# Kernel tuning notes

Hardware: AMD Instinct MI355X
Metric: run time of the kernel (lower is better)

The kernel has to match this reference:

```python
import jax, jax.numpy as jnp
import numpy as np
from jax import lax

D_MODEL = 1024
D_STATE = 16
D_CONV = 4
EXPAND = 2
D_INNER = EXPAND * D_MODEL
LN_EPS = 1e-5


def setup_inputs() -> dict:
    key = jax.random.key(0)
    ks = jax.random.split(key, 12)
    B, L = 4, 1024
    s = lambda fan_in: 1.0 / np.sqrt(fan_in)
    inp = {
        "x": jax.random.normal(ks[0], (B, L, D_MODEL), jnp.float32),
        # in_proj: d_model -> 2*d_inner (stored as (in, out))
        "W_in": jax.random.normal(ks[1], (D_MODEL, 2 * D_INNER), jnp.float32) * s(D_MODEL),
        "b_in": jnp.zeros((2 * D_INNER,), jnp.float32),
        # depthwise causal conv1d, kernel (d_inner, 1, d_conv)
        "conv_w": jax.random.normal(ks[2], (D_INNER, 1, D_CONV), jnp.float32) * s(D_CONV),
        "conv_b": jnp.zeros((D_INNER,), jnp.float32),
        # x_proj: d_inner -> 2*d_state
        "W_xp": jax.random.normal(ks[3], (D_INNER, 2 * D_STATE), jnp.float32) * s(D_INNER),
        "b_xp": jnp.zeros((2 * D_STATE,), jnp.float32),
        # dt_proj: d_inner -> d_inner
        "W_dt": jax.random.normal(ks[4], (D_INNER, D_INNER), jnp.float32) * s(D_INNER),
        "b_dt": jnp.zeros((D_INNER,), jnp.float32),
        # A_log = log(arange(1, d_state+1)) repeated over d_inner
        "A_log": jnp.log(jnp.broadcast_to(jnp.arange(1, D_STATE + 1, dtype=jnp.float32), (D_INNER, D_STATE))),
        "D_param": jnp.ones((D_INNER,), jnp.float32),
        # out_proj: d_inner -> d_model
        "W_out": jax.random.normal(ks[5], (D_INNER, D_MODEL), jnp.float32) * s(D_INNER),
        "b_out": jnp.zeros((D_MODEL,), jnp.float32),
        "ln_g": jnp.ones((D_MODEL,), jnp.float32),
        "ln_b": jnp.zeros((D_MODEL,), jnp.float32),
    }
    return inp


def _causal_depthwise_conv(x, w, b):
    # x: (B, d_inner, L); w: (d_inner, 1, d_conv). Left-pad d_conv-1 => causal.
    y = lax.conv_general_dilated(
        x, w, window_strides=(1,), padding=[(D_CONV - 1, 0)],
        dimension_numbers=("NCH", "OIH", "NCH"), feature_group_count=D_INNER)
    return y + b[None, :, None]


def _ssm(x, A, Bm, Cm, dt, D_param):
    # x, dt: (B,L,D)  A: (D,N)  Bm, Cm: (B,L,N)
    A_disc = jnp.exp(dt[..., None] * A)               # (B,L,D,N)
    dBx = (dt * x)[..., None] * Bm[:, :, None, :]     # (B,L,D,N) = dt*B*x_t
    h0 = jnp.zeros(x.shape[:1] + A.shape, x.dtype)    # (B,D,N)

    def step(h, inputs):
        a, bx, c = inputs                              # (B,D,N),(B,D,N),(B,N)
        h = a * h + bx
        y = jnp.einsum("bdn,bn->bd", h, c)
        return h, y

    _, ys = lax.scan(step, h0, (jnp.swapaxes(A_disc, 0, 1),
                                jnp.swapaxes(dBx, 0, 1),
                                jnp.swapaxes(Cm, 0, 1)))
    y = jnp.swapaxes(ys, 0, 1)                         # (B,L,D)
    return y + x * D_param


def reference(x, W_in, b_in, conv_w, conv_b, W_xp, b_xp, W_dt, b_dt,
              A_log, D_param, W_out, b_out, ln_g, ln_b):
    residual = x
    xr = x @ W_in + b_in                               # (B,L,2*d_inner)
    xi, res = jnp.split(xr, 2, axis=-1)
    xi = jax.nn.silu(xi)
    xi = jnp.swapaxes(xi, 1, 2)                        # (B,d_inner,L)
    xi = _causal_depthwise_conv(xi, conv_w, conv_b)
    xi = jnp.swapaxes(xi, 1, 2)
    xi = jax.nn.silu(xi)
    bc = xi @ W_xp + b_xp                              # (B,L,2*d_state)
    Bm, Cm = jnp.split(bc, 2, axis=-1)
    dt = jax.nn.softplus(xi @ W_dt + b_dt)
    A = -jnp.exp(A_log)                                # (d_inner, d_state)
    y = _ssm(xi, A, Bm, Cm, dt, D_param)
    y = y * jax.nn.silu(res)
    out = y @ W_out + b_out
    z = out + residual
    mu = jnp.mean(z, axis=-1, keepdims=True)
    var = jnp.var(z, axis=-1, keepdims=True)
    return (z - mu) * jax.lax.rsqrt(var + LN_EPS) * ln_g + ln_b
```

## Files before the change

### kernel.cpp

```cpp
#include <hip/hip_runtime.h>
#include <math.h>

#define D_MODEL 1024
#define D_INNER 2048
#define D_STATE 16
#define D_CONV  4
#define NCHUNK  16
#define LCHUNK  64

typedef unsigned short u16;
typedef __attribute__((ext_vector_type(8))) short short8;
typedef __attribute__((ext_vector_type(4))) float f32x4;
typedef __attribute__((ext_vector_type(4))) unsigned short u16x4;

__device__ __forceinline__ float silu_f(float x) { return x / (1.f + __expf(-x)); }
__device__ __forceinline__ float softplus_f(float x) {
    return fmaxf(x, 0.f) + log1pf(__expf(-fabsf(x)));
}
__device__ __forceinline__ u16 f2bf(float f) {
    union { float f; unsigned u; } c; c.f = f;
    unsigned r = c.u + 0x7fffu + ((c.u >> 16) & 1u);
    return (u16)(r >> 16);
}
__device__ __forceinline__ float bf2f(u16 v) {
    union { unsigned u; float f; } c; c.u = ((unsigned)v) << 16; return c.f;
}
__device__ __forceinline__ void gload_lds16(const void* g, void* l) {
    __builtin_amdgcn_global_load_lds((const __attribute__((address_space(1))) void*)g,
                                     (__attribute__((address_space(3))) void*)l, 16, 0, 0);
}

__global__ __launch_bounds__(256)
void f32_to_bf16_kernel(const float* __restrict__ in, u16* __restrict__ out, int n4)
{
    const int i = blockIdx.x * 256 + threadIdx.x;
    if (i >= n4) return;
    const float4 v = *(const float4*)&in[(size_t)i * 4];
    u16x4 o; o.x = f2bf(v.x); o.y = f2bf(v.y); o.z = f2bf(v.z); o.w = f2bf(v.w);
    *(u16x4*)&out[(size_t)i * 4] = o;
}

__global__ __launch_bounds__(256)
void transpose_bf16_kernel(const float* __restrict__ W, u16* __restrict__ Wt, int K, int N)
{
    __shared__ float tile[32][33];
    const int tx = threadIdx.x & 31, ty = threadIdx.x >> 5;
    const int n0 = blockIdx.x * 32, k0 = blockIdx.y * 32;
#pragma unroll
    for (int q = 0; q < 4; q++)
        tile[ty + q * 8][tx] = W[(size_t)(k0 + ty + q * 8) * N + n0 + tx];
    __syncthreads();
#pragma unroll
    for (int q = 0; q < 4; q++)
        Wt[(size_t)(n0 + ty + q * 8) * K + k0 + tx] = f2bf(tile[tx][ty + q * 8]);
}

template <int MODE>
__global__ __launch_bounds__(512, 2)
void gemm_mfma256(const u16* __restrict__ A, const u16* __restrict__ Bt,
                  const float* __restrict__ bias,
                  void* __restrict__ out0v, void* __restrict__ out1v,
                  int M, int N, int K)
{
    __shared__ __align__(16) short As[2][256 * 64];
    __shared__ __align__(16) short Bs[2][256 * 64];

    const int tid = threadIdx.x;
    const int wid = tid >> 6, lane = tid & 63;
    const int wr = wid >> 2, wc = wid & 3;
    const int row0 = blockIdx.y * 256, col0 = blockIdx.x * 256;
    const int kg = lane >> 4, r16 = lane & 15;

    f32x4 acc[8][4] = {};

    const u16* Abase = A + (size_t)row0 * K;
    const u16* Bbase = Bt + (size_t)col0 * K;

#define STAGE_A(bi, kk) do {                                                    \
        _Pragma("unroll")                                                       \
        for (int q = 0; q < 4; q++) {                                           \
            const int c = (q << 9) + tid;                                       \
            const int r = c >> 3;                                               \
            const int ks8 = (((c & 7) ^ (r & 7)) << 3);                         \
            gload_lds16(Abase + (size_t)r * K + (kk) + ks8,                     \
                        &As[bi][((q << 9) + (wid << 6)) << 3]);                 \
        }                                                                       \
    } while (0)
#define STAGE_B(bi, kk) do {                                                    \
        _Pragma("unroll")                                                       \
        for (int q = 0; q < 4; q++) {                                           \
            const int c = (q << 9) + tid;                                       \
            const int r = c >> 3;                                               \
            const int ks8 = (((c & 7) ^ (r & 7)) << 3);                         \
            gload_lds16(Bbase + (size_t)r * K + (kk) + ks8,                     \
                        &Bs[bi][((q << 9) + (wid << 6)) << 3]);                 \
        }                                                                       \
    } while (0)

    const int nt = K >> 6;
    STAGE_A(0, 0);
    STAGE_B(0, 0);

    int cur = 0;
    const int rx = r16 & 7;
    for (int t = 0; t < nt; ++t) {
        if (t + 1 < nt) {
            STAGE_A(cur ^ 1, (t + 1) << 6);
            asm volatile("s_waitcnt vmcnt(4)" ::: "memory");
        } else {
            asm volatile("s_waitcnt vmcnt(0)" ::: "memory");
        }
        __builtin_amdgcn_s_barrier();

#pragma unroll
        for (int ks = 0; ks < 2; ks++) {
            const int sl8 = (((ks << 2) + kg) ^ rx) << 3;
            short8 af[8], bg[4];
#pragma unroll
            for (int i = 0; i < 8; i++) {
                const int r = wr * 128 + i * 16 + r16;
                af[i] = *(const short8*)&As[cur][r * 64 + sl8];
            }
#pragma unroll
            for (int j = 0; j < 4; j++) {
                const int r = wc * 64 + j * 16 + r16;
                bg[j] = *(const short8*)&Bs[cur][r * 64 + sl8];
            }
            __builtin_amdgcn_s_setprio(1);
#pragma unroll
            for (int i = 0; i < 8; i++)
#pragma unroll
                for (int j = 0; j < 4; j++)
                    acc[i][j] = __builtin_amdgcn_mfma_f32_16x16x32_bf16(af[i], bg[j], acc[i][j], 0, 0, 0);
            __builtin_amdgcn_s_setprio(0);
            if (ks == 0 && t + 1 < nt)
                STAGE_B(cur ^ 1, (t + 1) << 6);
        }

        asm volatile("s_waitcnt lgkmcnt(0)" ::: "memory");
        __builtin_amdgcn_s_barrier();
        cur ^= 1;
    }
#undef STAGE_A
#undef STAGE_B

#pragma unroll
    for (int i = 0; i < 8; i++) {
#pragma unroll
        for (int j = 0; j < 4; j++) {
#pragma unroll
            for (int r = 0; r < 4; r++) {
                const int row = row0 + wr * 128 + i * 16 + kg * 4 + r;
                const int col = col0 + wc * 64 + j * 16 + r16;
                float v = acc[i][j][r] + bias[col];
                if (MODE == 0) {
                    u16* o0 = (u16*)out0v; u16* o1 = (u16*)out1v;
                    if (col < D_INNER) o0[(size_t)row * D_INNER + col] = f2bf(silu_f(v));
                    else               o1[(size_t)row * D_INNER + (col - D_INNER)] = f2bf(v);
                } else {
                    ((float*)out0v)[(size_t)row * N + col] = softplus_f(v);
                }
            }
        }
    }
}

template <int MODE>
__global__ __launch_bounds__(256)
void gemm_mfma_128(const u16* __restrict__ A, const u16* __restrict__ Bt,
                   const float* __restrict__ bias, const float* __restrict__ aux,
                   float* __restrict__ out0, int M, int N, int K)
{
    __shared__ __align__(16) short As[3][4096];
    __shared__ __align__(16) short Bs[3][4096];

    const int tid = threadIdx.x;
    const int wid = tid >> 6, lane = tid & 63;
    const int wr = wid >> 1, wc = wid & 1;
    const int row0 = blockIdx.y * 128, col0 = blockIdx.x * 128;

    f32x4 acc[4][4] = {};

    const int c0 = wid * 128 + lane;
    const int c1 = c0 + 64;
    const u16* Abase = A + (size_t)row0 * K;
    const u16* Bbase = Bt + (size_t)col0 * K;

    const int gsl8 = (((lane & 3) ^ ((lane >> 3) & 3)) << 3);
    const int kg = lane >> 4, r16 = lane & 15;
    const int sl8 = ((kg ^ ((r16 >> 1) & 3)) << 3);

#define STAGE(bi, kk) do {                                                                   \
        gload_lds16(Abase + (size_t)(c0 >> 2) * K + (kk) + gsl8, &As[bi][wid * 1024]);       \
        gload_lds16(Abase + (size_t)(c1 >> 2) * K + (kk) + gsl8, &As[bi][wid * 1024 + 512]); \
        gload_lds16(Bbase + (size_t)(c0 >> 2) * K + (kk) + gsl8, &Bs[bi][wid * 1024]);       \
        gload_lds16(Bbase + (size_t)(c1 >> 2) * K + (kk) + gsl8, &Bs[bi][wid * 1024 + 512]); \
    } while (0)

    const int nt = K >> 5;
    STAGE(0, 0);
    STAGE(1, 32);
    int cs = 0;
    for (int t = 0; t < nt; ++t) {
        if (t + 2 < nt) {
            const int ss = (cs + 2 >= 3) ? cs - 1 : cs + 2;
            STAGE(ss, (t + 2) << 5);
            asm volatile("s_waitcnt vmcnt(8)" ::: "memory");
        } else if (t + 1 < nt) {
            asm volatile("s_waitcnt vmcnt(4)" ::: "memory");
        } else {
            asm volatile("s_waitcnt vmcnt(0)" ::: "memory");
        }
        __builtin_amdgcn_s_barrier();

        short8 af[4], bg[4];
#pragma unroll
        for (int i = 0; i < 4; i++) {
            const int r = wr * 64 + i * 16 + r16;
            af[i] = *(const short8*)&As[cs][r * 32 + sl8];
        }
#pragma unroll
        for (int j = 0; j < 4; j++) {
            const int r = wc * 64 + j * 16 + r16;
            bg[j] = *(const short8*)&Bs[cs][r * 32 + sl8];
        }
        __builtin_amdgcn_s_setprio(1);
#pragma unroll
        for (int i = 0; i < 4; i++)
#pragma unroll
            for (int j = 0; j < 4; j++)
                acc[i][j] = __builtin_amdgcn_mfma_f32_16x16x32_bf16(af[i], bg[j], acc[i][j], 0, 0, 0);
        __builtin_amdgcn_s_setprio(0);

        asm volatile("s_waitcnt lgkmcnt(0)" ::: "memory");
        __builtin_amdgcn_s_barrier();
        cs = (cs + 1 >= 3) ? 0 : cs + 1;
    }
#undef STAGE

#pragma unroll
    for (int i = 0; i < 4; i++) {
#pragma unroll
        for (int j = 0; j < 4; j++) {
#pragma unroll
            for (int r = 0; r < 4; r++) {
                const int row = row0 + wr * 64 + i * 16 + kg * 4 + r;
                const int col = col0 + wc * 64 + j * 16 + r16;
                float v = acc[i][j][r] + bias[col];
                if (MODE == 1) out0[(size_t)row * N + col] = softplus_f(v);
                else           out0[(size_t)row * N + col] = v + aux[(size_t)row * N + col];
            }
        }
    }
}

__global__ __launch_bounds__(256)
void conv_silu_kernel(const u16* __restrict__ xi, const float* __restrict__ w,
                      const float* __restrict__ cb, float* __restrict__ xc,
                      u16* __restrict__ xcb, int total)
{
    const int i = blockIdx.x * 256 + threadIdx.x;
    if (i >= total) return;
    const int d = i & (D_INNER - 1);
    const int l = (i >> 11) & 1023;
    float acc = cb[d];
#pragma unroll
    for (int k = 0; k < D_CONV; k++) {
        const int li = l + k - (D_CONV - 1);
        if (li >= 0) acc = fmaf(w[d * D_CONV + k], bf2f(xi[(size_t)i + (k - (D_CONV - 1)) * D_INNER]), acc);
    }
    const float s = silu_f(acc);
    xc[i] = s;
    xcb[i] = f2bf(s);
}

__global__ __launch_bounds__(256)
void xproj_mfma_kernel(const u16* __restrict__ A, const u16* __restrict__ Wt,
                       const float* __restrict__ bxp, float* __restrict__ bc)
{
    const int wid = threadIdx.x >> 6, lane = threadIdx.x & 63;
    const int kg = lane >> 4, r16 = lane & 15;
    const int tok0 = blockIdx.x * 64 + wid * 16;

    f32x4 acc[2] = {};
#pragma unroll 4
    for (int k0 = 0; k0 < D_INNER; k0 += 32) {
        const short8 a  = *(const short8*)&A[(size_t)(tok0 + r16) * D_INNER + k0 + kg * 8];
        const short8 b0 = *(const short8*)&Wt[(size_t)r16 * D_INNER + k0 + kg * 8];
        const short8 b1 = *(const short8*)&Wt[(size_t)(16 + r16) * D_INNER + k0 + kg * 8];
        acc[0] = __builtin_amdgcn_mfma_f32_16x16x32_bf16(a, b0, acc[0], 0, 0, 0);
        acc[1] = __builtin_amdgcn_mfma_f32_16x16x32_bf16(a, b1, acc[1], 0, 0, 0);
    }
#pragma unroll
    for (int j = 0; j < 2; j++)
#pragma unroll
        for (int r = 0; r < 4; r++) {
            const int token = tok0 + kg * 4 + r;
            const int c = j * 16 + r16;
            bc[(size_t)token * 32 + c] = acc[j][r] + bxp[c];
        }
}

__global__ __launch_bounds__(256)
void ssm_s1_kernel(const float* __restrict__ xc, const float* __restrict__ dt,
                   const float* __restrict__ bc, const float* __restrict__ A_log,
                   float* __restrict__ hend, float* __restrict__ dtsum)
{
    const int tid = threadIdx.x;
    const int ch = tid >> 4, n = tid & 15;
    const int d0 = blockIdx.x * 16;
    const int c = blockIdx.y;
    const int b = blockIdx.z;
    const int d = d0 + ch;

    const float Aln = -__expf(A_log[d * D_STATE + n]);

    __shared__ float sdt[64][16], sdtx[64][16], sB[64][16];

    float h = 0.f, S = 0.f;

    const int l0 = c * LCHUNK;
    {
        const int l = tid >> 2, di = (tid & 3) << 2;
        const size_t g = ((size_t)(b * 1024 + l0 + l)) * D_INNER + d0 + di;
        const float4 dv = *(const float4*)&dt[g];
        const float4 xv = *(const float4*)&xc[g];
        float4 dx;
        dx.x = dv.x * xv.x; dx.y = dv.y * xv.y; dx.z = dv.z * xv.z; dx.w = dv.w * xv.w;
        *(float4*)&sdt[l][di] = dv;
        *(float4*)&sdtx[l][di] = dx;
        *(float4*)&sB[l][di] = *(const float4*)&bc[((size_t)(b * 1024 + l0 + l)) * 32 + di];
    }
    __syncthreads();
#pragma unroll 16
    for (int l = 0; l < 64; l++) {
        const float dtv = sdt[l][ch];
        const float a = __expf(dtv * Aln);
        h = fmaf(a, h, sdtx[l][ch] * sB[l][n]);
        S += dtv;
    }
    hend[((size_t)(b * NCHUNK + c) * D_INNER + d) * D_STATE + n] = h;
    if (n == 0) dtsum[(size_t)(b * NCHUNK + c) * D_INNER + d] = S;
}

__global__ __launch_bounds__(256)
void ssm_s3_kernel(const float* __restrict__ xc, const float* __restrict__ dt,
                   const float* __restrict__ bc, const float* __restrict__ A_log,
                   const float* __restrict__ Dp, const u16* __restrict__ resbf,
                   const float* __restrict__ hend, const float* __restrict__ dtsum,
                   u16* __restrict__ ybf)
{
    const int tid = threadIdx.x;
    const int wid = tid >> 6, lane = tid & 63;
    const int ch4 = lane >> 4, n = lane & 15;
    const int ch = wid * 4 + ch4;
    const int d0 = blockIdx.x * 16;
    const int c = blockIdx.y;
    const int b = blockIdx.z;
    const int d = d0 + ch;

    const float Aln = -__expf(A_log[d * D_STATE + n]);
    const float Dv = Dp[d];

    float h = 0.f;
    for (int cc = 0; cc < c; cc++) {
        const float S = dtsum[(size_t)(b * NCHUNK + cc) * D_INNER + d];
        const float P = __expf(Aln * S);
        h = fmaf(P, h, hend[((size_t)(b * NCHUNK + cc) * D_INNER + d) * D_STATE + n]);
    }

    __shared__ float sdt[64][16], sdtx[64][16], sx[64][16], sres[64][16];
    __shared__ float sbc[64][32];
    __shared__ float pbuf[4 * 16 * 68];

    float* pw = &pbuf[wid * 16 * 68];

    const int l0 = c * LCHUNK;
    {
        const int l = tid >> 2, di = (tid & 3) << 2;
        const size_t g = ((size_t)(b * 1024 + l0 + l)) * D_INNER + d0 + di;
        const float4 dv = *(const float4*)&dt[g];
        const float4 xv = *(const float4*)&xc[g];
        const u16x4 rv = *(const u16x4*)&resbf[g];
        float4 dx;
        dx.x = dv.x * xv.x; dx.y = dv.y * xv.y; dx.z = dv.z * xv.z; dx.w = dv.w * xv.w;
        *(float4*)&sdt[l][di] = dv;
        *(float4*)&sdtx[l][di] = dx;
        *(float4*)&sx[l][di] = xv;
        sres[l][di + 0] = bf2f(rv.x);
        sres[l][di + 1] = bf2f(rv.y);
        sres[l][di + 2] = bf2f(rv.z);
        sres[l][di + 3] = bf2f(rv.w);
        const int r0 = tid >> 3, c4 = (tid & 7) << 2;
        *(float4*)&sbc[r0][c4] = *(const float4*)&bc[((size_t)(b * 1024 + l0 + r0)) * 32 + c4];
        const int r1 = (tid + 256) >> 3;
        *(float4*)&sbc[r1][c4] = *(const float4*)&bc[((size_t)(b * 1024 + l0 + r1)) * 32 + c4];
    }
    __syncthreads();

    for (int l16 = 0; l16 < 4; l16++) {
#pragma unroll
        for (int j = 0; j < 16; j++) {
            const int l = l16 * 16 + j;
            const float dtv = sdt[l][ch];
            const float a = __expf(dtv * Aln);
            h = fmaf(a, h, sdtx[l][ch] * sbc[l][n]);
            pw[j * 68 + ch4 * 16 + n] = h * sbc[l][16 + n];
        }
        __builtin_amdgcn_wave_barrier();
        const float4 q0 = *(const float4*)&pw[n * 68 + ch4 * 16 + 0];
        const float4 q1 = *(const float4*)&pw[n * 68 + ch4 * 16 + 4];
        const float4 q2 = *(const float4*)&pw[n * 68 + ch4 * 16 + 8];
        const float4 q3 = *(const float4*)&pw[n * 68 + ch4 * 16 + 12];
        const float sum = ((q0.x + q0.y) + (q0.z + q0.w)) + ((q1.x + q1.y) + (q1.z + q1.w))
                        + ((q2.x + q2.y) + (q2.z + q2.w)) + ((q3.x + q3.y) + (q3.z + q3.w));
        const int t = l16 * 16 + n;
        const float xv = sx[t][ch];
        const float rv = sres[t][ch];
        const float yv = (sum + xv * Dv) * silu_f(rv);
        ybf[((size_t)(b * 1024 + l0 + t)) * D_INNER + d] = f2bf(yv);
        __builtin_amdgcn_wave_barrier();
    }
}

__global__ __launch_bounds__(256)
void layernorm_kernel(const float* __restrict__ z, const float* __restrict__ g,
                      const float* __restrict__ beta, float* __restrict__ out)
{
    const int row = blockIdx.x;
    const int tid = threadIdx.x;
    const float* zr = z + (size_t)row * D_MODEL;
    const float4 v = *(const float4*)&zr[tid << 2];
    float s = v.x + v.y + v.z + v.w;
    float ss = v.x * v.x + v.y * v.y + v.z * v.z + v.w * v.w;

    __shared__ float sm[256], sq[256];
    sm[tid] = s; sq[tid] = ss;
    __syncthreads();
    for (int off = 128; off > 0; off >>= 1) {
        if (tid < off) { sm[tid] += sm[tid + off]; sq[tid] += sq[tid + off]; }
        __syncthreads();
    }
    const float mean = sm[0] * (1.f / D_MODEL);
    const float var = sq[0] * (1.f / D_MODEL) - mean * mean;
    const float rstd = rsqrtf(var + 1e-5f);

    float4 o;
    o.x = (v.x - mean) * rstd * g[(tid << 2) + 0] + beta[(tid << 2) + 0];
    o.y = (v.y - mean) * rstd * g[(tid << 2) + 1] + beta[(tid << 2) + 1];
    o.z = (v.z - mean) * rstd * g[(tid << 2) + 2] + beta[(tid << 2) + 2];
    o.w = (v.w - mean) * rstd * g[(tid << 2) + 3] + beta[(tid << 2) + 3];
    *(float4*)&out[(size_t)row * D_MODEL + (tid << 2)] = o;
}

extern "C" void kernel_launch(void* const* d_in, const int* in_sizes, int n_in,
                              void* d_out, int out_size, void* d_ws, size_t ws_size,
                              hipStream_t stream)
{
    const float* x      = (const float*)d_in[0];
    const float* W_in   = (const float*)d_in[1];
    const float* b_in   = (const float*)d_in[2];
    const float* conv_w = (const float*)d_in[3];
    const float* conv_b = (const float*)d_in[4];
    const float* W_xp   = (const float*)d_in[5];
    const float* b_xp   = (const float*)d_in[6];
    const float* W_dt   = (const float*)d_in[7];
    const float* b_dt   = (const float*)d_in[8];
    const float* A_log  = (const float*)d_in[9];
    const float* D_par  = (const float*)d_in[10];
    const float* W_out  = (const float*)d_in[11];
    const float* b_out  = (const float*)d_in[12];
    const float* ln_g   = (const float*)d_in[13];
    const float* ln_b   = (const float*)d_in[14];
    float* out = (float*)d_out;

    const int BL = in_sizes[0] / D_MODEL;
    const int Bb = BL / 1024;
    const size_t BLD = (size_t)BL * D_INNER;

    float* ws    = (float*)d_ws;
    float* xcb   = ws;
    float* dtb   = xcb + BLD;
    float* bcbuf = dtb + BLD;
    float* hend  = bcbuf + (size_t)BL * 32;
    float* dtsum = hend + (size_t)Bb * NCHUNK * D_INNER * D_STATE;
    u16*   xibf  = (u16*)(dtsum + (size_t)Bb * NCHUNK * D_INNER);
    u16*   resbf = xibf + BLD;
    u16*   xcbf  = resbf + BLD;
    u16*   xbf   = xcbf + BLD;
    u16*   wxpT  = xbf + (size_t)BL * D_MODEL;
    u16*   wtmp  = wxpT + 32 * D_INNER;
    u16*   ybf   = xibf;
    float* zbuf  = dtb;

    f32_to_bf16_kernel<<<(BL * D_MODEL / 4 + 255) / 256, 256, 0, stream>>>(x, xbf, BL * D_MODEL / 4);

    transpose_bf16_kernel<<<dim3(2 * D_INNER / 32, D_MODEL / 32), 256, 0, stream>>>(W_in, wtmp, D_MODEL, 2 * D_INNER);

    gemm_mfma256<0><<<dim3(2 * D_INNER / 256, BL / 256), 512, 0, stream>>>(
        xbf, wtmp, b_in, xibf, resbf, BL, 2 * D_INNER, D_MODEL);

    transpose_bf16_kernel<<<dim3(1, D_INNER / 32), 256, 0, stream>>>(W_xp, wxpT, D_INNER, 32);

    conv_silu_kernel<<<(int)(BLD / 256), 256, 0, stream>>>(
        xibf, conv_w, conv_b, xcb, xcbf, (int)BLD);

    xproj_mfma_kernel<<<BL / 64, 256, 0, stream>>>(xcbf, wxpT, b_xp, bcbuf);

    transpose_bf16_kernel<<<dim3(D_INNER / 32, D_INNER / 32), 256, 0, stream>>>(W_dt, wtmp, D_INNER, D_INNER);

    gemm_mfma_128<1><<<dim3(D_INNER / 128, BL / 128), 256, 0, stream>>>(
        xcbf, wtmp, b_dt, nullptr, dtb, BL, D_INNER, D_INNER);

    ssm_s1_kernel<<<dim3(D_INNER / 16, NCHUNK, Bb), 256, 0, stream>>>(
        xcb, dtb, bcbuf, A_log, hend, dtsum);

    ssm_s3_kernel<<<dim3(D_INNER / 16, NCHUNK, Bb), 256, 0, stream>>>(
        xcb, dtb, bcbuf, A_log, D_par, resbf, hend, dtsum, ybf);

    transpose_bf16_kernel<<<dim3(D_MODEL / 32, D_INNER / 32), 256, 0, stream>>>(W_out, wtmp, D_INNER, D_MODEL);

    gemm_mfma_128<2><<<dim3(D_MODEL / 128, BL / 128), 256, 0, stream>>>(
        ybf, wtmp, b_out, x, zbuf, BL, D_MODEL, D_INNER);

    layernorm_kernel<<<BL, 256, 0, stream>>>(zbuf, ln_g, ln_b, out);
}
```

Baseline: 359.1 us.

## Restructure chunked SSM scan: per-channel threads, separate carry pass, bf16 conv output

Each SSM thread now owns one channel and holds all 16 state values in registers, reading dt and bf16 x straight from global memory with coalesced per-token loads. The cross-chunk carry is moved into its own s2 kernel instead of having every s3 block redo the prefix over earlier chunks. Chunks shrink from 64 to 32 tokens, the fp32 conv output buffer is dropped in favour of the existing bf16 one, and the conv kernel now handles 8 channels per thread with vector loads. In exchange, x is read at bf16 precision in the scan, per-thread register use goes up, blocks have less parallelism per block, and there is one extra kernel launch.

```diff
diff --git a/kernel.cpp b/kernel.cpp
--- a/kernel.cpp
+++ b/kernel.cpp
@@ -5,13 +5,14 @@
 #define D_INNER 2048
 #define D_STATE 16
 #define D_CONV  4
-#define NCHUNK  16
-#define LCHUNK  64
+#define NCHUNK  32
+#define LCHUNK  32
 
 typedef unsigned short u16;
 typedef __attribute__((ext_vector_type(8))) short short8;
 typedef __attribute__((ext_vector_type(4))) float f32x4;
 typedef __attribute__((ext_vector_type(4))) unsigned short u16x4;
+typedef __attribute__((ext_vector_type(8))) unsigned short u16x8;
 
 __device__ __forceinline__ float silu_f(float x) { return x / (1.f + __expf(-x)); }
 __device__ __forceinline__ float softplus_f(float x) {
@@ -255,23 +256,40 @@
 }
 
 __global__ __launch_bounds__(256)
-void conv_silu_kernel(const u16* __restrict__ xi, const float* __restrict__ w,
-                      const float* __restrict__ cb, float* __restrict__ xc,
-                      u16* __restrict__ xcb, int total)
+void conv_silu8_kernel(const u16* __restrict__ xi, const float* __restrict__ w,
+                       const float* __restrict__ cb, u16* __restrict__ xcb, int total8)
 {
     const int i = blockIdx.x * 256 + threadIdx.x;
-    if (i >= total) return;
-    const int d = i & (D_INNER - 1);
-    const int l = (i >> 11) & 1023;
-    float acc = cb[d];
+    if (i >= total8) return;
+    const size_t i8 = (size_t)i * 8;
+    const int d8 = (int)(i8 & (D_INNER - 1));
+    const int l = (int)((i8 >> 11) & 1023);
+
+    float acc[8];
+#pragma unroll
+    for (int c = 0; c < 8; c++) acc[c] = cb[d8 + c];
+
+    float4 wv[8];
+#pragma unroll
+    for (int c = 0; c < 8; c++) wv[c] = *(const float4*)&w[(d8 + c) * 4];
+
 #pragma unroll
     for (int k = 0; k < D_CONV; k++) {
-        const int li = l + k - (D_CONV - 1);
-        if (li >= 0) acc = fmaf(w[d * D_CONV + k], bf2f(xi[(size_t)i + (k - (D_CONV - 1)) * D_INNER]), acc);
-    }
-    const float s = silu_f(acc);
-    xc[i] = s;
-    xcb[i] = f2bf(s);
+        if (l + k - (D_CONV - 1) >= 0) {
+            const u16x8 v = *(const u16x8*)&xi[i8 + (size_t)(k - (D_CONV - 1)) * D_INNER];
+            const float wk0 = ((const float*)&wv[0])[k];
+#pragma unroll
+            for (int c = 0; c < 8; c++) {
+                const float wk = ((const float*)&wv[c])[k];
+                acc[c] = fmaf(wk, bf2f(v[c]), acc[c]);
+            }
+            (void)wk0;
+        }
+    }
+    u16x8 o;
+#pragma unroll
+    for (int c = 0; c < 8; c++) o[c] = f2bf(silu_f(acc[c]));
+    *(u16x8*)&xcb[i8] = o;
 }
 
 __global__ __launch_bounds__(256)
@@ -302,124 +320,139 @@
 }
 
 __global__ __launch_bounds__(256)
-void ssm_s1_kernel(const float* __restrict__ xc, const float* __restrict__ dt,
+void ssm_s1_kernel(const u16* __restrict__ xcbf, const float* __restrict__ dt,
                    const float* __restrict__ bc, const float* __restrict__ A_log,
                    float* __restrict__ hend, float* __restrict__ dtsum)
 {
     const int tid = threadIdx.x;
-    const int ch = tid >> 4, n = tid & 15;
-    const int d0 = blockIdx.x * 16;
+    const int d = blockIdx.x * 256 + tid;
     const int c = blockIdx.y;
     const int b = blockIdx.z;
-    const int d = d0 + ch;
-
-    const float Aln = -__expf(A_log[d * D_STATE + n]);
-
-    __shared__ float sdt[64][16], sdtx[64][16], sB[64][16];
-
-    float h = 0.f, S = 0.f;
-
-    const int l0 = c * LCHUNK;
+
+    __shared__ float sB[LCHUNK][16];
     {
-        const int l = tid >> 2, di = (tid & 3) << 2;
-        const size_t g = ((size_t)(b * 1024 + l0 + l)) * D_INNER + d0 + di;
-        const float4 dv = *(const float4*)&dt[g];
-        const float4 xv = *(const float4*)&xc[g];
-        float4 dx;
-        dx.x = dv.x * xv.x; dx.y = dv.y * xv.y; dx.z = dv.z * xv.z; dx.w = dv.w * xv.w;
-        *(float4*)&sdt[l][di] = dv;
-        *(float4*)&sdtx[l][di] = dx;
-        *(float4*)&sB[l][di] = *(const float4*)&bc[((size_t)(b * 1024 + l0 + l)) * 32 + di];
-    }
+        if (tid < LCHUNK * 4) {
+            const int row = tid >> 2, c4 = (tid & 3) << 2;
+            *(float4*)&sB[row][c4] = *(const float4*)&bc[((size_t)(b * 1024 + c * LCHUNK + row)) * 32 + c4];
+        }
+    }
+
+    float Aln[D_STATE];
+#pragma unroll
+    for (int q = 0; q < 4; q++) {
+        const f32x4 a = *(const f32x4*)&A_log[(size_t)d * D_STATE + q * 4];
+        Aln[q * 4 + 0] = -__expf(a.x); Aln[q * 4 + 1] = -__expf(a.y);
+        Aln[q * 4 + 2] = -__expf(a.z); Aln[q * 4 + 3] = -__expf(a.w);
+    }
+
+    const size_t base = ((size_t)(b * 1024 + c * LCHUNK)) * D_INNER + d;
+    const float* dtp = dt + base;
+    const u16* xp = xcbf + base;
+
+    float h[D_STATE] = {};
+    float S = 0.f;
     __syncthreads();
+
 #pragma unroll 16
-    for (int l = 0; l < 64; l++) {
-        const float dtv = sdt[l][ch];
-        const float a = __expf(dtv * Aln);
-        h = fmaf(a, h, sdtx[l][ch] * sB[l][n]);
-        S += dtv;
-    }
-    hend[((size_t)(b * NCHUNK + c) * D_INNER + d) * D_STATE + n] = h;
-    if (n == 0) dtsum[(size_t)(b * NCHUNK + c) * D_INNER + d] = S;
-}
-
-__global__ __launch_bounds__(256)
-void ssm_s3_kernel(const float* __restrict__ xc, const float* __restrict__ dt,
+    for (int j = 0; j < LCHUNK; j++) {
+        const float dtf = dtp[(size_t)j * D_INNER];
+        const float xf = bf2f(xp[(size_t)j * D_INNER]);
+        const float dtx = dtf * xf;
+        S += dtf;
+#pragma unroll
+        for (int n = 0; n < D_STATE; n++) {
+            const float a = __expf(dtf * Aln[n]);
+            h[n] = fmaf(a, h[n], dtx * sB[j][n]);
+        }
+    }
+
+    const size_t ob = ((size_t)(b * NCHUNK + c) * D_INNER + d);
+#pragma unroll
+    for (int q = 0; q < 4; q++) {
+        f32x4 hv = {h[q * 4 + 0], h[q * 4 + 1], h[q * 4 + 2], h[q * 4 + 3]};
+        *(f32x4*)&hend[ob * D_STATE + q * 4] = hv;
+    }
+    dtsum[ob] = S;
+}
+
+__global__ __launch_bounds__(256)
+void ssm_s2_kernel(const float* __restrict__ hend, const float* __restrict__ dtsum,
+                   const float* __restrict__ A_log, float* __restrict__ hin)
+{
+    const int tid = threadIdx.x;
+    const int d = blockIdx.x * 16 + (tid >> 4);
+    const int n = tid & 15;
+    const int b = blockIdx.y;
+
+    const float Aln = -__expf(A_log[(size_t)d * D_STATE + n]);
+    float h = 0.f;
+#pragma unroll
+    for (int c = 0; c < NCHUNK; c++) {
+        const size_t ob = ((size_t)(b * NCHUNK + c) * D_INNER + d);
+        hin[ob * D_STATE + n] = h;
+        const float P = __expf(Aln * dtsum[ob]);
+        h = fmaf(P, h, hend[ob * D_STATE + n]);
+    }
+}
+
+__global__ __launch_bounds__(256)
+void ssm_s3_kernel(const u16* __restrict__ xcbf, const float* __restrict__ dt,
                    const float* __restrict__ bc, const float* __restrict__ A_log,
                    const float* __restrict__ Dp, const u16* __restrict__ resbf,
-                   const float* __restrict__ hend, const float* __restrict__ dtsum,
-                   u16* __restrict__ ybf)
+                   const float* __restrict__ hin, u16* __restrict__ ybf)
 {
     const int tid = threadIdx.x;
-    const int wid = tid >> 6, lane = tid & 63;
-    const int ch4 = lane >> 4, n = lane & 15;
-    const int ch = wid * 4 + ch4;
-    const int d0 = blockIdx.x * 16;
+    const int d = blockIdx.x * 256 + tid;
     const int c = blockIdx.y;
     const int b = blockIdx.z;
-    const int d = d0 + ch;
-
-    const float Aln = -__expf(A_log[d * D_STATE + n]);
+
+    __shared__ float sbc[LCHUNK][32];
+    {
+        const int row = tid >> 3, c4 = (tid & 7) << 2;
+        if (row < LCHUNK)
+            *(float4*)&sbc[row][c4] = *(const float4*)&bc[((size_t)(b * 1024 + c * LCHUNK + row)) * 32 + c4];
+    }
+
+    float Aln[D_STATE];
+#pragma unroll
+    for (int q = 0; q < 4; q++) {
+        const f32x4 a = *(const f32x4*)&A_log[(size_t)d * D_STATE + q * 4];
+        Aln[q * 4 + 0] = -__expf(a.x); Aln[q * 4 + 1] = -__expf(a.y);
+        Aln[q * 4 + 2] = -__expf(a.z); Aln[q * 4 + 3] = -__expf(a.w);
+    }
     const float Dv = Dp[d];
 
-    float h = 0.f;
-    for (int cc = 0; cc < c; cc++) {
-        const float S = dtsum[(size_t)(b * NCHUNK + cc) * D_INNER + d];
-        const float P = __expf(Aln * S);
-        h = fmaf(P, h, hend[((size_t)(b * NCHUNK + cc) * D_INNER + d) * D_STATE + n]);
-    }
-
-    __shared__ float sdt[64][16], sdtx[64][16], sx[64][16], sres[64][16];
-    __shared__ float sbc[64][32];
-    __shared__ float pbuf[4 * 16 * 68];
-
-    float* pw = &pbuf[wid * 16 * 68];
-
-    const int l0 = c * LCHUNK;
-    {
-        const int l = tid >> 2, di = (tid & 3) << 2;
-        const size_t g = ((size_t)(b * 1024 + l0 + l)) * D_INNER + d0 + di;
-        const float4 dv = *(const float4*)&dt[g];
-        const float4 xv = *(const float4*)&xc[g];
-        const u16x4 rv = *(const u16x4*)&resbf[g];
-        float4 dx;
-        dx.x = dv.x * xv.x; dx.y = dv.y * xv.y; dx.z = dv.z * xv.z; dx.w = dv.w * xv.w;
-        *(float4*)&sdt[l][di] = dv;
-        *(float4*)&sdtx[l][di] = dx;
-        *(float4*)&sx[l][di] = xv;
-        sres[l][di + 0] = bf2f(rv.x);
-        sres[l][di + 1] = bf2f(rv.y);
-        sres[l][di + 2] = bf2f(rv.z);
-        sres[l][di + 3] = bf2f(rv.w);
-        const int r0 = tid >> 3, c4 = (tid & 7) << 2;
-        *(float4*)&sbc[r0][c4] = *(const float4*)&bc[((size_t)(b * 1024 + l0 + r0)) * 32 + c4];
-        const int r1 = (tid + 256) >> 3;
-        *(float4*)&sbc[r1][c4] = *(const float4*)&bc[((size_t)(b * 1024 + l0 + r1)) * 32 + c4];
-    }
+    float h[D_STATE];
+    const size_t ob = ((size_t)(b * NCHUNK + c) * D_INNER + d);
+#pragma unroll
+    for (int q = 0; q < 4; q++) {
+        const f32x4 hv = *(const f32x4*)&hin[ob * D_STATE + q * 4];
+        h[q * 4 + 0] = hv.x; h[q * 4 + 1] = hv.y; h[q * 4 + 2] = hv.z; h[q * 4 + 3] = hv.w;
+    }
+
+    const size_t base = ((size_t)(b * 1024 + c * LCHUNK)) * D_INNER + d;
+    const float* dtp = dt + base;
+    const u16* xp = xcbf + base;
+    const u16* rp = resbf + base;
+    u16* yp = ybf + base;
+
     __syncthreads();
 
-    for (int l16 = 0; l16 < 4; l16++) {
-#pragma unroll
-        for (int j = 0; j < 16; j++) {
-            const int l = l16 * 16 + j;
-            const float dtv = sdt[l][ch];
-            const float a = __expf(dtv * Aln);
-            h = fmaf(a, h, sdtx[l][ch] * sbc[l][n]);
-            pw[j * 68 + ch4 * 16 + n] = h * sbc[l][16 + n];
-        }
-        __builtin_amdgcn_wave_barrier();
-        const float4 q0 = *(const float4*)&pw[n * 68 + ch4 * 16 + 0];
-        const float4 q1 = *(const float4*)&pw[n * 68 + ch4 * 16 + 4];
-        const float4 q2 = *(const float4*)&pw[n * 68 + ch4 * 16 + 8];
-        const float4 q3 = *(const float4*)&pw[n * 68 + ch4 * 16 + 12];
-        const float sum = ((q0.x + q0.y) + (q0.z + q0.w)) + ((q1.x + q1.y) + (q1.z + q1.w))
-                        + ((q2.x + q2.y) + (q2.z + q2.w)) + ((q3.x + q3.y) + (q3.z + q3.w));
-        const int t = l16 * 16 + n;
-        const float xv = sx[t][ch];
-        const float rv = sres[t][ch];
-        const float yv = (sum + xv * Dv) * silu_f(rv);
-        ybf[((size_t)(b * 1024 + l0 + t)) * D_INNER + d] = f2bf(yv);
-        __builtin_amdgcn_wave_barrier();
+#pragma unroll 16
+    for (int j = 0; j < LCHUNK; j++) {
+        const float dtf = dtp[(size_t)j * D_INNER];
+        const float xf = bf2f(xp[(size_t)j * D_INNER]);
+        const float rf = bf2f(rp[(size_t)j * D_INNER]);
+        const float dtx = dtf * xf;
+        float yv = 0.f;
+#pragma unroll
+        for (int n = 0; n < D_STATE; n++) {
+            const float a = __expf(dtf * Aln[n]);
+            h[n] = fmaf(a, h[n], dtx * sbc[j][n]);
+            yv = fmaf(h[n], sbc[j][16 + n], yv);
+        }
+        yv = (yv + xf * Dv) * silu_f(rf);
+        yp[(size_t)j * D_INNER] = f2bf(yv);
     }
 }
 
@@ -479,12 +512,12 @@
     const size_t BLD = (size_t)BL * D_INNER;
 
     float* ws    = (float*)d_ws;
-    float* xcb   = ws;
-    float* dtb   = xcb + BLD;
+    float* dtb   = ws;
     float* bcbuf = dtb + BLD;
     float* hend  = bcbuf + (size_t)BL * 32;
     float* dtsum = hend + (size_t)Bb * NCHUNK * D_INNER * D_STATE;
-    u16*   xibf  = (u16*)(dtsum + (size_t)Bb * NCHUNK * D_INNER);
+    float* hinb  = dtsum + (size_t)Bb * NCHUNK * D_INNER;
+    u16*   xibf  = (u16*)(hinb + (size_t)Bb * NCHUNK * D_INNER * D_STATE);
     u16*   resbf = xibf + BLD;
     u16*   xcbf  = resbf + BLD;
     u16*   xbf   = xcbf + BLD;
@@ -502,8 +535,8 @@
 
     transpose_bf16_kernel<<<dim3(1, D_INNER / 32), 256, 0, stream>>>(W_xp, wxpT, D_INNER, 32);
 
-    conv_silu_kernel<<<(int)(BLD / 256), 256, 0, stream>>>(
-        xibf, conv_w, conv_b, xcb, xcbf, (int)BLD);
+    conv_silu8_kernel<<<(int)(BLD / 8 / 256), 256, 0, stream>>>(
+        xibf, conv_w, conv_b, xcbf, (int)(BLD / 8));
 
     xproj_mfma_kernel<<<BL / 64, 256, 0, stream>>>(xcbf, wxpT, b_xp, bcbuf);
 
@@ -512,11 +545,14 @@
     gemm_mfma_128<1><<<dim3(D_INNER / 128, BL / 128), 256, 0, stream>>>(
         xcbf, wtmp, b_dt, nullptr, dtb, BL, D_INNER, D_INNER);
 
-    ssm_s1_kernel<<<dim3(D_INNER / 16, NCHUNK, Bb), 256, 0, stream>>>(
-        xcb, dtb, bcbuf, A_log, hend, dtsum);
-
-    ssm_s3_kernel<<<dim3(D_INNER / 16, NCHUNK, Bb), 256, 0, stream>>>(
-        xcb, dtb, bcbuf, A_log, D_par, resbf, hend, dtsum, ybf);
+    ssm_s1_kernel<<<dim3(D_INNER / 256, NCHUNK, Bb), 256, 0, stream>>>(
+        xcbf, dtb, bcbuf, A_log, hend, dtsum);
+
+    ssm_s2_kernel<<<dim3(D_INNER / 16, Bb), 256, 0, stream>>>(
+        hend, dtsum, A_log, hinb);
+
+    ssm_s3_kernel<<<dim3(D_INNER / 256, NCHUNK, Bb), 256, 0, stream>>>(
+        xcbf, dtb, bcbuf, A_log, D_par, resbf, hinb, ybf);
 
     transpose_bf16_kernel<<<dim3(D_MODEL / 32, D_INNER / 32), 256, 0, stream>>>(W_out, wtmp, D_INNER, D_MODEL);
 
```

Result: faster. 327.9 us (-8.7%).
